# Optimization experiments

Hardware: AMD Instinct MI355X
Metric: run time of the kernel (lower is better)

Reference implementation:

```python
import jax, jax.numpy as jnp
import numpy as np

B, T, H, V = 64, 512, 300, 50257


def setup_inputs() -> dict:
    key = jax.random.key(0)
    k0, k1, k2, k3, k4 = jax.random.split(key, 5)
    tokens = jax.random.randint(k0, (B, T), 0, V, dtype=jnp.int32)
    ihs = jnp.zeros((B, H), jnp.float32)
    emb = jax.random.normal(k1, (V, H), jnp.float32) * 0.02
    W = jax.random.normal(k2, (H, H), jnp.float32) * (1.0 / np.sqrt(H))
    U = jax.random.normal(k3, (H, H), jnp.float32) * (1.0 / np.sqrt(H))
    Wout = jax.random.normal(k4, (V, H), jnp.float32) * 0.02
    bout = jnp.zeros((V,), jnp.float32)
    return {"ihs": ihs, "tokens": tokens, "emb": emb, "W": W, "U": U,
            "Wout": Wout, "bout": bout}


def reference(ihs, tokens, emb, W, U, Wout, bout):
    # Embedding lookup: [B, T, H]
    x = emb[tokens]
    # Precompute input projection for all timesteps: U x_t (Linear: x @ U^T)
    ux = jnp.einsum('bth,gh->btg', x, U)  # [B, T, H]
    ux_tmajor = jnp.swapaxes(ux, 0, 1)    # [T, B, H]

    def step(h, ux_t):
        # h_t = tanh(W h_{t-1} + U x_t)
        h_next = jnp.tanh(h @ W.T + ux_t)
        return h_next, h_next

    h_last, _ = jax.lax.scan(step, ihs, ux_tmajor)
    # final hidden state -> vocab logits
    logits = h_last @ Wout.T + bout  # [B, V]
    return logits
```

## Files before the change

kernel.cpp:

```cpp
#include <hip/hip_runtime.h>
#include <math.h>

#define H 300
#define BB 64
#define TT 512
#define VV 50257
#define KC 30

__global__ void transpose_k(const float* __restrict__ in, float* __restrict__ out) {
    int idx = blockIdx.x * blockDim.x + threadIdx.x;
    if (idx < H * H) {
        int r = idx / H, c = idx - r * H;
        out[idx] = in[c * H + r];
    }
}

__global__ __launch_bounds__(256) void ux_k(const int* __restrict__ tokens,
                                            const float* __restrict__ emb,
                                            const float* __restrict__ Ut,
                                            float* __restrict__ ux) {
    __shared__ __align__(16) float x_s[KC][BB];
    __shared__ __align__(16) float ut_s[KC][304];
    __shared__ int tok_s[BB];

    const int t = blockIdx.x;
    const int tid = threadIdx.x;
    if (tid < BB) tok_s[tid] = tokens[tid * TT + t];

    const int tb = tid >> 4;
    const int tg = tid & 15;
    const int b0 = tb * 4;
    const int g0 = tg * 20;
    const bool active = (tg < 15);

    float acc[4][20];
#pragma unroll
    for (int i = 0; i < 4; ++i)
#pragma unroll
        for (int j = 0; j < 20; ++j) acc[i][j] = 0.f;

    __syncthreads();

    for (int h0 = 0; h0 < H; h0 += KC) {
        for (int i = tid; i < BB * 32; i += 256) {
            int b = i >> 5, k = i & 31;
            if (k < KC) x_s[k][b] = emb[tok_s[b] * H + h0 + k];
        }
        for (int i = tid; i < KC * H; i += 256) {
            int k = i / H, g = i - k * H;
            ut_s[k][g] = Ut[(h0 + k) * H + g];
        }
        __syncthreads();
        if (active) {
#pragma unroll 2
            for (int k = 0; k < KC; ++k) {
                float4 xa = *reinterpret_cast<const float4*>(&x_s[k][b0]);
                float4 u0 = *reinterpret_cast<const float4*>(&ut_s[k][g0 + 0]);
                float4 u1 = *reinterpret_cast<const float4*>(&ut_s[k][g0 + 4]);
                float4 u2 = *reinterpret_cast<const float4*>(&ut_s[k][g0 + 8]);
                float4 u3 = *reinterpret_cast<const float4*>(&ut_s[k][g0 + 12]);
                float4 u4 = *reinterpret_cast<const float4*>(&ut_s[k][g0 + 16]);
                const float xr[4] = {xa.x, xa.y, xa.z, xa.w};
                const float ur[20] = {u0.x, u0.y, u0.z, u0.w,
                                      u1.x, u1.y, u1.z, u1.w,
                                      u2.x, u2.y, u2.z, u2.w,
                                      u3.x, u3.y, u3.z, u3.w,
                                      u4.x, u4.y, u4.z, u4.w};
#pragma unroll
                for (int i = 0; i < 4; ++i)
#pragma unroll
                    for (int j = 0; j < 20; ++j)
                        acc[i][j] += xr[i] * ur[j];
            }
        }
        __syncthreads();
    }

    if (active) {
#pragma unroll
        for (int i = 0; i < 4; ++i) {
            float* dst = ux + (t * BB + b0 + i) * H + g0;
#pragma unroll
            for (int jq = 0; jq < 5; ++jq) {
                *reinterpret_cast<float4*>(dst + jq * 4) =
                    make_float4(acc[i][jq * 4 + 0], acc[i][jq * 4 + 1],
                                acc[i][jq * 4 + 2], acc[i][jq * 4 + 3]);
            }
        }
    }
}

#define RNN_REP19(X) X(0) X(1) X(2) X(3) X(4) X(5) X(6) X(7) X(8) X(9) \
    X(10) X(11) X(12) X(13) X(14) X(15) X(16) X(17) X(18)

__global__ __attribute__((amdgpu_flat_work_group_size(512, 512), amdgpu_waves_per_eu(2, 2)))
void rnn_k(const float* __restrict__ W,
           const float* __restrict__ ux,
           const float* __restrict__ ihs,
           float* __restrict__ hlast) {
    __shared__ __align__(16) float4 wl4_s[450 * 11];
    __shared__ __align__(16) float h_s[304];
    __shared__ float p_s[608];
    const int b = blockIdx.x;
    const int tid = threadIdx.x;
    const int tt = (tid < 450) ? tid : 449;
    const int c = tt / 150;
    const int g2 = tt - c * 150;

    const float4* wrA4 = reinterpret_cast<const float4*>(W + (size_t)g2 * H + c * 100);
    const float4* wrB4 = reinterpret_cast<const float4*>(W + (size_t)(g2 + 150) * H + c * 100);

#define RNN_WA(q) float4 wa##q = wrA4[q];
    RNN_REP19(RNN_WA)
#undef RNN_WA
#define RNN_WB(q) float4 wb##q = wrB4[q];
    RNN_REP19(RNN_WB)
#undef RNN_WB
    float4 wb19 = wrB4[19];

    const int wbase = tt * 11;
#pragma unroll
    for (int i = 0; i < 6; ++i) wl4_s[wbase + i] = wrA4[19 + i];
#pragma unroll
    for (int i = 0; i < 5; ++i) wl4_s[wbase + 6 + i] = wrB4[20 + i];

    if (tid < H) h_s[tid] = ihs[b * H + tid];

    const float* uxb = ux + b * H;
    float u0 = 0.f, u1 = 0.f;
    if (tid < 150) {
        u0 = uxb[g2];
        u1 = uxb[150 + g2];
    }
    __syncthreads();

    const float4* hs4 = reinterpret_cast<const float4*>(h_s);
    const int hoff = c * 25;

#pragma unroll 1
    for (int t = 0; t < TT; ++t) {
        float n0 = 0.f, n1 = 0.f;
        if (tid < 150 && t + 1 < TT) {
            const float* nx = uxb + (t + 1) * (BB * H);
            n0 = nx[g2];
            n1 = nx[150 + g2];
        }
        float accA0 = 0.f, accA1 = 0.f, accA2 = 0.f, accA3 = 0.f;
        float accB0 = 0.f, accB1 = 0.f, accB2 = 0.f, accB3 = 0.f;
#define RNN_Q(q) { float4 h4 = hs4[hoff + q]; \
        accA0 += wa##q.x * h4.x; accA1 += wa##q.y * h4.y; \
        accA2 += wa##q.z * h4.z; accA3 += wa##q.w * h4.w; \
        accB0 += wb##q.x * h4.x; accB1 += wb##q.y * h4.y; \
        accB2 += wb##q.z * h4.z; accB3 += wb##q.w * h4.w; }
        RNN_REP19(RNN_Q)
#undef RNN_Q
        {
            float4 h4 = hs4[hoff + 19];
            float4 wA = wl4_s[wbase + 0];
            accA0 += wA.x * h4.x; accA1 += wA.y * h4.y;
            accA2 += wA.z * h4.z; accA3 += wA.w * h4.w;
            accB0 += wb19.x * h4.x; accB1 += wb19.y * h4.y;
            accB2 += wb19.z * h4.z; accB3 += wb19.w * h4.w;
        }
#pragma unroll
        for (int q = 20; q < 25; ++q) {
            float4 h4 = hs4[hoff + q];
            float4 wA = wl4_s[wbase + (q - 19)];
            float4 wB = wl4_s[wbase + 6 + (q - 20)];
            accA0 += wA.x * h4.x; accA1 += wA.y * h4.y;
            accA2 += wA.z * h4.z; accA3 += wA.w * h4.w;
            accB0 += wB.x * h4.x; accB1 += wB.y * h4.y;
            accB2 += wB.z * h4.z; accB3 += wB.w * h4.w;
        }
        float accA = (accA0 + accA1) + (accA2 + accA3);
        float accB = (accB0 + accB1) + (accB2 + accB3);
        if (tid < 450 && c == 1) { p_s[g2] = accA; p_s[150 + g2] = accB; }
        if (tid < 450 && c == 2) { p_s[304 + g2] = accA; p_s[454 + g2] = accB; }
        __syncthreads();
        if (tid < 150) {
            float z0 = accA + p_s[g2] + p_s[304 + g2] + u0;
            float z1 = accB + p_s[150 + g2] + p_s[454 + g2] + u1;
            float e0 = __expf(2.f * z0);
            float e1 = __expf(2.f * z1);
            h_s[g2]       = 1.f - 2.f * __builtin_amdgcn_rcpf(e0 + 1.f);
            h_s[150 + g2] = 1.f - 2.f * __builtin_amdgcn_rcpf(e1 + 1.f);
        }
        u0 = n0; u1 = n1;
        __syncthreads();
    }
    if (tid < H) hlast[b * H + tid] = h_s[tid];
}

__global__ __launch_bounds__(256) void logits_k(const float* __restrict__ hlast,
                                                const float* __restrict__ Wout,
                                                const float* __restrict__ bout,
                                                float* __restrict__ out) {
    __shared__ __align__(16) float Ws[32 * 132];
    __shared__ __align__(16) float hs[32 * 76];
    const int tid = threadIdx.x;
    const int tv = tid & 31;
    const int tb = tid >> 5;
    const int v0 = blockIdx.x * 128;

    float acc[8][4];
#pragma unroll
    for (int i = 0; i < 8; ++i)
#pragma unroll
        for (int j = 0; j < 4; ++j) acc[i][j] = 0.f;

    for (int hb = 0; hb < H; hb += 32) {
        __syncthreads();
        {
            const int vp = tid >> 1;
            const int hloc = (tid & 1) * 16;
            int vv = v0 + vp; if (vv > VV - 1) vv = VV - 1;
            const float* wrow = Wout + (size_t)vv * H + hb + hloc;
#pragma unroll
            for (int i = 0; i < 4; ++i) {
                const int hg = hb + hloc + i * 4;
                float4 val;
                if (hg + 3 < H) {
                    val = *reinterpret_cast<const float4*>(wrow + i * 4);
                } else {
                    val.x = (hg + 0 < H) ? wrow[i * 4 + 0] : 0.f;
                    val.y = (hg + 1 < H) ? wrow[i * 4 + 1] : 0.f;
                    val.z = (hg + 2 < H) ? wrow[i * 4 + 2] : 0.f;
                    val.w = (hg + 3 < H) ? wrow[i * 4 + 3] : 0.f;
                }
                Ws[(hloc + i * 4 + 0) * 132 + vp] = val.x;
                Ws[(hloc + i * 4 + 1) * 132 + vp] = val.y;
                Ws[(hloc + i * 4 + 2) * 132 + vp] = val.z;
                Ws[(hloc + i * 4 + 3) * 132 + vp] = val.w;
            }
        }
        {
            const int bb = tid >> 2;
            const int hl = (tid & 3) * 8;
            const float* hrow = hlast + bb * H + hb + hl;
#pragma unroll
            for (int i = 0; i < 2; ++i) {
                const int hg = hb + hl + i * 4;
                float4 val;
                if (hg + 3 < H) {
                    val = *reinterpret_cast<const float4*>(hrow + i * 4);
                } else {
                    val.x = (hg + 0 < H) ? hrow[i * 4 + 0] : 0.f;
                    val.y = (hg + 1 < H) ? hrow[i * 4 + 1] : 0.f;
                    val.z = (hg + 2 < H) ? hrow[i * 4 + 2] : 0.f;
                    val.w = (hg + 3 < H) ? hrow[i * 4 + 3] : 0.f;
                }
                hs[(hl + i * 4 + 0) * 76 + bb] = val.x;
                hs[(hl + i * 4 + 1) * 76 + bb] = val.y;
                hs[(hl + i * 4 + 2) * 76 + bb] = val.z;
                hs[(hl + i * 4 + 3) * 76 + bb] = val.w;
            }
        }
        __syncthreads();
        const float4* Ws4 = reinterpret_cast<const float4*>(Ws);
        const float4* hs4 = reinterpret_cast<const float4*>(hs);
#pragma unroll
        for (int h2 = 0; h2 < 32; ++h2) {
            float4 w4  = Ws4[h2 * 33 + tv];
            float4 h4a = hs4[h2 * 19 + tb * 2];
            float4 h4b = hs4[h2 * 19 + tb * 2 + 1];
            const float hv[8] = {h4a.x, h4a.y, h4a.z, h4a.w,
                                 h4b.x, h4b.y, h4b.z, h4b.w};
#pragma unroll
            for (int bi = 0; bi < 8; ++bi) {
                acc[bi][0] += hv[bi] * w4.x;
                acc[bi][1] += hv[bi] * w4.y;
                acc[bi][2] += hv[bi] * w4.z;
                acc[bi][3] += hv[bi] * w4.w;
            }
        }
    }

    const int vg = v0 + tv * 4;
    float4 bq;
    if (vg + 3 < VV) bq = *reinterpret_cast<const float4*>(bout + vg);
    else {
        bq.x = (vg + 0 < VV) ? bout[vg + 0] : 0.f;
        bq.y = (vg + 1 < VV) ? bout[vg + 1] : 0.f;
        bq.z = (vg + 2 < VV) ? bout[vg + 2] : 0.f;
        bq.w = (vg + 3 < VV) ? bout[vg + 3] : 0.f;
    }
#pragma unroll
    for (int bi = 0; bi < 8; ++bi) {
        const int bb = tb * 8 + bi;
        float* op = out + (size_t)bb * VV + vg;
        if (vg + 0 < VV) op[0] = acc[bi][0] + bq.x;
        if (vg + 1 < VV) op[1] = acc[bi][1] + bq.y;
        if (vg + 2 < VV) op[2] = acc[bi][2] + bq.z;
        if (vg + 3 < VV) op[3] = acc[bi][3] + bq.w;
    }
}

extern "C" void kernel_launch(void* const* d_in, const int* in_sizes, int n_in,
                              void* d_out, int out_size, void* d_ws, size_t ws_size,
                              hipStream_t stream) {
    const float* ihs    = (const float*)d_in[0];
    const int*   tokens = (const int*)  d_in[1];
    const float* emb    = (const float*)d_in[2];
    const float* W      = (const float*)d_in[3];
    const float* U      = (const float*)d_in[4];
    const float* Wout   = (const float*)d_in[5];
    const float* bout   = (const float*)d_in[6];
    float* out = (float*)d_out;

    char* ws = (char*)d_ws;
    float* Ut    = (float*)(ws + 0);
    float* hlast = (float*)(ws + 400000);
    float* ux    = (float*)(ws + 1048576);

    const int tp_blocks = (H * H + 255) / 256;
    transpose_k<<<tp_blocks, 256, 0, stream>>>(U, Ut);
    ux_k<<<TT, 256, 0, stream>>>(tokens, emb, Ut, ux);
    rnn_k<<<BB, 512, 0, stream>>>(W, ux, ihs, hlast);
    logits_k<<<(VV + 127) / 128, 256, 0, stream>>>(hlast, Wout, bout, out);
}
```

Before: 810.6 us.

## Repartition RNN recurrence into 5 K-chunks with 3 rows per thread, all weights in registers

The recurrent matvec work is split so that 500 threads each handle 3 output rows over a 60-wide K chunk (5 chunks), instead of 450 threads handling 2 rows over 100-wide chunks. This keeps the whole W slice in registers (180 floats) and removes the LDS spill of leftover weights, so each step reads only h from LDS. In exchange the partial-sum reduction grows to 4 LDS partials per output, register pressure is high, and a large unused shared pool is declared that may limit occupancy.

```diff
diff --git a/kernel.cpp b/kernel.cpp
--- a/kernel.cpp
+++ b/kernel.cpp
@@ -90,102 +90,94 @@
     }
 }
 
-#define RNN_REP19(X) X(0) X(1) X(2) X(3) X(4) X(5) X(6) X(7) X(8) X(9) \
-    X(10) X(11) X(12) X(13) X(14) X(15) X(16) X(17) X(18)
+#define RNN_Q15(X) X(0) X(1) X(2) X(3) X(4) X(5) X(6) X(7) X(8) X(9) \
+    X(10) X(11) X(12) X(13) X(14)
 
 __global__ __attribute__((amdgpu_flat_work_group_size(512, 512), amdgpu_waves_per_eu(2, 2)))
 void rnn_k(const float* __restrict__ W,
            const float* __restrict__ ux,
            const float* __restrict__ ihs,
            float* __restrict__ hlast) {
-    __shared__ __align__(16) float4 wl4_s[450 * 11];
-    __shared__ __align__(16) float h_s[304];
-    __shared__ float p_s[608];
+    __shared__ __align__(16) float shpool[20800];
+    float* h_s = shpool;
+    float* p_s = shpool + 304;
+
     const int b = blockIdx.x;
     const int tid = threadIdx.x;
-    const int tt = (tid < 450) ? tid : 449;
-    const int c = tt / 150;
-    const int g2 = tt - c * 150;
-
-    const float4* wrA4 = reinterpret_cast<const float4*>(W + (size_t)g2 * H + c * 100);
-    const float4* wrB4 = reinterpret_cast<const float4*>(W + (size_t)(g2 + 150) * H + c * 100);
-
-#define RNN_WA(q) float4 wa##q = wrA4[q];
-    RNN_REP19(RNN_WA)
-#undef RNN_WA
-#define RNN_WB(q) float4 wb##q = wrB4[q];
-    RNN_REP19(RNN_WB)
-#undef RNN_WB
-    float4 wb19 = wrB4[19];
-
-    const int wbase = tt * 11;
-#pragma unroll
-    for (int i = 0; i < 6; ++i) wl4_s[wbase + i] = wrA4[19 + i];
-#pragma unroll
-    for (int i = 0; i < 5; ++i) wl4_s[wbase + 6 + i] = wrB4[20 + i];
+    const int tt = (tid < 500) ? tid : 499;
+    const int c  = tt / 100;
+    const int g3 = tt - c * 100;
+
+    const float4* w0p = reinterpret_cast<const float4*>(W + (size_t)(g3      ) * H + c * 60);
+    const float4* w1p = reinterpret_cast<const float4*>(W + (size_t)(g3 + 100) * H + c * 60);
+    const float4* w2p = reinterpret_cast<const float4*>(W + (size_t)(g3 + 200) * H + c * 60);
+
+#define RNN_DW(q) float4 w0_##q = w0p[q]; float4 w1_##q = w1p[q]; float4 w2_##q = w2p[q];
+    RNN_Q15(RNN_DW)
+#undef RNN_DW
 
     if (tid < H) h_s[tid] = ihs[b * H + tid];
 
-    const float* uxb = ux + b * H;
-    float u0 = 0.f, u1 = 0.f;
-    if (tid < 150) {
-        u0 = uxb[g2];
-        u1 = uxb[150 + g2];
+    const float* uxb = ux + (size_t)b * H;
+    float u0 = 0.f, u1 = 0.f, u2 = 0.f;
+    if (tid < 100) {
+        u0 = uxb[g3];
+        u1 = uxb[100 + g3];
+        u2 = uxb[200 + g3];
     }
     __syncthreads();
 
     const float4* hs4 = reinterpret_cast<const float4*>(h_s);
-    const int hoff = c * 25;
+    const int c15 = c * 15;
 
 #pragma unroll 1
     for (int t = 0; t < TT; ++t) {
-        float n0 = 0.f, n1 = 0.f;
-        if (tid < 150 && t + 1 < TT) {
-            const float* nx = uxb + (t + 1) * (BB * H);
-            n0 = nx[g2];
-            n1 = nx[150 + g2];
-        }
-        float accA0 = 0.f, accA1 = 0.f, accA2 = 0.f, accA3 = 0.f;
-        float accB0 = 0.f, accB1 = 0.f, accB2 = 0.f, accB3 = 0.f;
-#define RNN_Q(q) { float4 h4 = hs4[hoff + q]; \
-        accA0 += wa##q.x * h4.x; accA1 += wa##q.y * h4.y; \
-        accA2 += wa##q.z * h4.z; accA3 += wa##q.w * h4.w; \
-        accB0 += wb##q.x * h4.x; accB1 += wb##q.y * h4.y; \
-        accB2 += wb##q.z * h4.z; accB3 += wb##q.w * h4.w; }
-        RNN_REP19(RNN_Q)
-#undef RNN_Q
-        {
-            float4 h4 = hs4[hoff + 19];
-            float4 wA = wl4_s[wbase + 0];
-            accA0 += wA.x * h4.x; accA1 += wA.y * h4.y;
-            accA2 += wA.z * h4.z; accA3 += wA.w * h4.w;
-            accB0 += wb19.x * h4.x; accB1 += wb19.y * h4.y;
-            accB2 += wb19.z * h4.z; accB3 += wb19.w * h4.w;
-        }
-#pragma unroll
-        for (int q = 20; q < 25; ++q) {
-            float4 h4 = hs4[hoff + q];
-            float4 wA = wl4_s[wbase + (q - 19)];
-            float4 wB = wl4_s[wbase + 6 + (q - 20)];
-            accA0 += wA.x * h4.x; accA1 += wA.y * h4.y;
-            accA2 += wA.z * h4.z; accA3 += wA.w * h4.w;
-            accB0 += wB.x * h4.x; accB1 += wB.y * h4.y;
-            accB2 += wB.z * h4.z; accB3 += wB.w * h4.w;
-        }
-        float accA = (accA0 + accA1) + (accA2 + accA3);
-        float accB = (accB0 + accB1) + (accB2 + accB3);
-        if (tid < 450 && c == 1) { p_s[g2] = accA; p_s[150 + g2] = accB; }
-        if (tid < 450 && c == 2) { p_s[304 + g2] = accA; p_s[454 + g2] = accB; }
-        __syncthreads();
-        if (tid < 150) {
-            float z0 = accA + p_s[g2] + p_s[304 + g2] + u0;
-            float z1 = accB + p_s[150 + g2] + p_s[454 + g2] + u1;
+        float n0 = 0.f, n1 = 0.f, n2 = 0.f;
+        if (tid < 100 && t + 1 < TT) {
+            const float* nx = uxb + (size_t)(t + 1) * (BB * H);
+            n0 = nx[g3];
+            n1 = nx[100 + g3];
+            n2 = nx[200 + g3];
+        }
+        float4 a0 = make_float4(0.f, 0.f, 0.f, 0.f);
+        float4 a1 = make_float4(0.f, 0.f, 0.f, 0.f);
+        float4 a2 = make_float4(0.f, 0.f, 0.f, 0.f);
+#define RNN_FMA(q) { float4 h4 = hs4[c15 + q]; \
+        a0.x += w0_##q.x * h4.x; a0.y += w0_##q.y * h4.y; \
+        a0.z += w0_##q.z * h4.z; a0.w += w0_##q.w * h4.w; \
+        a1.x += w1_##q.x * h4.x; a1.y += w1_##q.y * h4.y; \
+        a1.z += w1_##q.z * h4.z; a1.w += w1_##q.w * h4.w; \
+        a2.x += w2_##q.x * h4.x; a2.y += w2_##q.y * h4.y; \
+        a2.z += w2_##q.z * h4.z; a2.w += w2_##q.w * h4.w; }
+        RNN_Q15(RNN_FMA)
+#undef RNN_FMA
+        float pA0 = (a0.x + a0.y) + (a0.z + a0.w);
+        float pA1 = (a1.x + a1.y) + (a1.z + a1.w);
+        float pA2 = (a2.x + a2.y) + (a2.z + a2.w);
+        if (tid < 500 && c != 0) {
+            p_s[(c - 1) * 304 + g3      ] = pA0;
+            p_s[(c - 1) * 304 + g3 + 100] = pA1;
+            p_s[(c - 1) * 304 + g3 + 200] = pA2;
+        }
+        __syncthreads();
+        if (tid < 100) {
+            float z0 = pA0 + u0;
+            float z1 = pA1 + u1;
+            float z2 = pA2 + u2;
+#pragma unroll
+            for (int j = 0; j < 4; ++j) {
+                z0 += p_s[j * 304 + g3];
+                z1 += p_s[j * 304 + g3 + 100];
+                z2 += p_s[j * 304 + g3 + 200];
+            }
             float e0 = __expf(2.f * z0);
             float e1 = __expf(2.f * z1);
-            h_s[g2]       = 1.f - 2.f * __builtin_amdgcn_rcpf(e0 + 1.f);
-            h_s[150 + g2] = 1.f - 2.f * __builtin_amdgcn_rcpf(e1 + 1.f);
-        }
-        u0 = n0; u1 = n1;
+            float e2 = __expf(2.f * z2);
+            h_s[g3      ] = 1.f - 2.f * __builtin_amdgcn_rcpf(e0 + 1.f);
+            h_s[g3 + 100] = 1.f - 2.f * __builtin_amdgcn_rcpf(e1 + 1.f);
+            h_s[g3 + 200] = 1.f - 2.f * __builtin_amdgcn_rcpf(e2 + 1.f);
+        }
+        u0 = n0; u1 = n1; u2 = n2;
         __syncthreads();
     }
     if (tid < H) hlast[b * H + tid] = h_s[tid];
```

New measurement: 715.7 us. 1.13x faster.
